# Kernel optimization log

Measured on AMD Instinct MI355X. Metric: run time of the kernel, lower is better.

## Reference

```python
import jax, jax.numpy as jnp
import numpy as np

N = 8192
IN_F = 512
OUT_F = 64
ALPHA = 0.2  # LeakyReLU negative slope
NEG_INF = -9e15


def setup_inputs() -> dict:
    key = jax.random.key(0)
    k1, k2, k3, k4 = jax.random.split(key, 4)
    inp = jax.random.normal(k1, (N, IN_F), dtype=jnp.float32)
    adj = jax.random.randint(k2, (N, N), 0, 2, dtype=jnp.int32)
    W = jax.random.normal(k3, (IN_F, OUT_F), dtype=jnp.float32) * (1.414 * (6.0 / (IN_F + OUT_F)) ** 0.5)
    a = jax.random.normal(k4, (2 * OUT_F, 1), dtype=jnp.float32) * (1.414 * (6.0 / (2 * OUT_F + 1)) ** 0.5)
    return {"input": inp, "adj": adj, "W": W, "a": a}


def reference(input, adj, W, a):
    h = input @ W                      # [N, F]
    F_ = h.shape[1]
    # e_ij = leakyrelu(a[:F].h_i + a[F:].h_j)  (equivalent to the concat form)
    f_src = h @ a[:F_, 0]              # [N]
    f_dst = h @ a[F_:, 0]              # [N]
    e = jax.nn.leaky_relu(f_src[:, None] + f_dst[None, :], negative_slope=ALPHA)  # [N, N]
    att = jnp.where(adj > 0, e, jnp.float32(NEG_INF))
    att = jax.nn.softmax(att, axis=1)  # dropout p is inert in eval mode
    h_prime = att @ h                  # [N, F]
    return jax.nn.elu(h_prime)         # concat=True
```

## Files before the change

kernel.cpp:

```cpp
#include <hip/hip_runtime.h>

#define N_NODES 8192
#define IN_F 512
#define OUT_F 64
#define LOG2E 1.4426950408889634f

typedef short bf16x8 __attribute__((ext_vector_type(8)));
typedef float f32x4 __attribute__((ext_vector_type(4)));
typedef int i32x4 __attribute__((ext_vector_type(4)));

__global__ __launch_bounds__(256) void k_gemm(const float* __restrict__ input,
                                              const float* __restrict__ W,
                                              const float* __restrict__ a,
                                              unsigned short* __restrict__ hT,
                                              float* __restrict__ fsrcL,
                                              float* __restrict__ fdstL) {
  const int lane = threadIdx.x & 63;
  const int wv = threadIdx.x >> 6;
  const int r0 = blockIdx.x * 4;
  const int row = r0 + wv;
  const float* inrow = input + (size_t)row * IN_F;
  const int c = lane;
  float acc = 0.f;
  for (int k = 0; k < IN_F; k += 4) {
    float4 x = *(const float4*)(inrow + k);
    acc += x.x * W[(k + 0) * OUT_F + c];
    acc += x.y * W[(k + 1) * OUT_F + c];
    acc += x.z * W[(k + 2) * OUT_F + c];
    acc += x.w * W[(k + 3) * OUT_F + c];
  }
  float vs = acc * a[c];
  float vd = acc * a[OUT_F + c];
#pragma unroll
  for (int off = 32; off > 0; off >>= 1) {
    vs += __shfl_xor(vs, off, 64);
    vd += __shfl_xor(vd, off, 64);
  }
  if (lane == 0) {
    fsrcL[row] = vs * LOG2E;
    fdstL[row] = vd * LOG2E;
  }
  __shared__ float hs[4][64];
  hs[wv][c] = acc;
  __syncthreads();
  if (threadIdx.x < 64) {
    const int cc = threadIdx.x;
    unsigned u0 = __float_as_uint(hs[0][cc]) + 0x8000u;
    unsigned u1 = __float_as_uint(hs[1][cc]) + 0x8000u;
    unsigned u2 = __float_as_uint(hs[2][cc]) + 0x8000u;
    unsigned u3 = __float_as_uint(hs[3][cc]) + 0x8000u;
    uint2 pk;
    pk.x = __builtin_amdgcn_perm(u1, u0, 0x07060302u);
    pk.y = __builtin_amdgcn_perm(u3, u2, 0x07060302u);
    *(uint2*)(hT + (size_t)cc * N_NODES + r0) = pk;
  }
}

__global__ __launch_bounds__(256) void k_prep(const float* __restrict__ fdstL,
                                              float* __restrict__ ML,
                                              float* __restrict__ E1,
                                              float* __restrict__ E2) {
  float m = -3.0e38f;
  for (int i = threadIdx.x; i < N_NODES; i += 256) {
    float v = fdstL[i];
    E1[i] = __builtin_amdgcn_exp2f(v);
    E2[i] = __builtin_amdgcn_exp2f(0.2f * v);
    m = fmaxf(m, v);
  }
#pragma unroll
  for (int off = 32; off > 0; off >>= 1) m = fmaxf(m, __shfl_xor(m, off, 64));
  __shared__ float sm[4];
  if ((threadIdx.x & 63) == 0) sm[threadIdx.x >> 6] = m;
  __syncthreads();
  if (threadIdx.x == 0) ML[0] = fmaxf(fmaxf(sm[0], sm[1]), fmaxf(sm[2], sm[3]));
}

__global__ __launch_bounds__(512) void k_attn(const int* __restrict__ adj,
                                              const unsigned short* __restrict__ hT,
                                              const float* __restrict__ fsrcL,
                                              const float* __restrict__ MLp,
                                              const float* __restrict__ E1,
                                              const float* __restrict__ E2,
                                              float* __restrict__ out) {
  const int lane = threadIdx.x & 63;
  const int wv = threadIdx.x >> 6;
  const int i0 = blockIdx.x * 16;
  const int m = lane & 15;
  const int g = lane >> 4;

  const float MLv = MLp[0];
  const float fs = fsrcL[i0 + m];
  const float xm = fs + MLv;
  const float mL = fmaxf(xm, 0.2f * xm);
  const float S1 = __builtin_amdgcn_exp2f(fs - mL);
  const float S2 = __builtin_amdgcn_exp2f(0.2f * fs - mL);
  const float Ti = __builtin_amdgcn_exp2f(-fs);

  f32x4 acc0{}, acc1{}, acc2{}, acc3{}, acc4{};
  union { unsigned w[4]; bf16x8 v; } ones;
  ones.w[0] = ones.w[1] = ones.w[2] = ones.w[3] = 0x3F803F80u;

  const int* adjrow = adj + (size_t)(i0 + m) * N_NODES;
  const unsigned short* hT0 = hT + (size_t)m * N_NODES;

  const int jbeg = wv * (N_NODES / 8);
  for (int j0 = jbeg; j0 < jbeg + (N_NODES / 8); j0 += 64) {
#pragma unroll
    for (int s = 0; s < 2; s++) {
      const int jb = j0 + s * 32 + g * 8;
      i32x4 a0 = __builtin_nontemporal_load((const i32x4*)(adjrow + jb));
      i32x4 a1 = __builtin_nontemporal_load((const i32x4*)(adjrow + jb) + 1);
      float4 e1a = *(const float4*)(E1 + jb);
      float4 e1b = *(const float4*)(E1 + jb + 4);
      float4 e2a = *(const float4*)(E2 + jb);
      float4 e2b = *(const float4*)(E2 + jb + 4);
      bf16x8 b0 = *(const bf16x8*)(hT0 + jb);
      bf16x8 b1 = *(const bf16x8*)(hT0 + (size_t)16 * N_NODES + jb);
      bf16x8 b2 = *(const bf16x8*)(hT0 + (size_t)32 * N_NODES + jb);
      bf16x8 b3 = *(const bf16x8*)(hT0 + (size_t)48 * N_NODES + jb);

      const int av[8] = {a0.x, a0.y, a0.z, a0.w, a1.x, a1.y, a1.z, a1.w};
      const float e1v[8] = {e1a.x, e1a.y, e1a.z, e1a.w, e1b.x, e1b.y, e1b.z, e1b.w};
      const float e2v[8] = {e2a.x, e2a.y, e2a.z, e2a.w, e2b.x, e2b.y, e2b.z, e2b.w};
      unsigned u[8];
#pragma unroll
      for (int t = 0; t < 8; t++) {
        float p = (e1v[t] >= Ti) ? e1v[t] * S1 : e2v[t] * S2;
        p = av[t] ? p : 0.0f;
        u[t] = __float_as_uint(p) + 0x8000u;
      }
      union { unsigned w[4]; bf16x8 v; } pc;
      pc.w[0] = __builtin_amdgcn_perm(u[1], u[0], 0x07060302u);
      pc.w[1] = __builtin_amdgcn_perm(u[3], u[2], 0x07060302u);
      pc.w[2] = __builtin_amdgcn_perm(u[5], u[4], 0x07060302u);
      pc.w[3] = __builtin_amdgcn_perm(u[7], u[6], 0x07060302u);

      acc0 = __builtin_amdgcn_mfma_f32_16x16x32_bf16(pc.v, b0, acc0, 0, 0, 0);
      acc1 = __builtin_amdgcn_mfma_f32_16x16x32_bf16(pc.v, b1, acc1, 0, 0, 0);
      acc2 = __builtin_amdgcn_mfma_f32_16x16x32_bf16(pc.v, b2, acc2, 0, 0, 0);
      acc3 = __builtin_amdgcn_mfma_f32_16x16x32_bf16(pc.v, b3, acc3, 0, 0, 0);
      acc4 = __builtin_amdgcn_mfma_f32_16x16x32_bf16(pc.v, ones.v, acc4, 0, 0, 0);
    }
  }

  __shared__ float accbuf[8][16][64];
  __shared__ float lbuf[8][16];
#pragma unroll
  for (int r = 0; r < 4; r++) {
    accbuf[wv][g * 4 + r][0 + m]  = acc0[r];
    accbuf[wv][g * 4 + r][16 + m] = acc1[r];
    accbuf[wv][g * 4 + r][32 + m] = acc2[r];
    accbuf[wv][g * 4 + r][48 + m] = acc3[r];
  }
  if ((lane & 15) == 0) {
#pragma unroll
    for (int r = 0; r < 4; r++) lbuf[wv][g * 4 + r] = acc4[r];
  }
  __syncthreads();

#pragma unroll
  for (int q = 0; q < 2; q++) {
    int idx = q * 512 + threadIdx.x;
    int r = idx >> 6, c = idx & 63;
    float ssum = 0.f, l = 0.f;
#pragma unroll
    for (int w = 0; w < 8; w++) {
      ssum += accbuf[w][r][c];
      l += lbuf[w][r];
    }
    float v = ssum / l;
    out[(size_t)(i0 + r) * OUT_F + c] =
        v > 0.f ? v : __builtin_amdgcn_exp2f(v * LOG2E) - 1.f;
  }
}

extern "C" void kernel_launch(void* const* d_in, const int* in_sizes, int n_in,
                              void* d_out, int out_size, void* d_ws, size_t ws_size,
                              hipStream_t stream) {
  const float* input = (const float*)d_in[0];
  const int* adj = (const int*)d_in[1];
  const float* W = (const float*)d_in[2];
  const float* a = (const float*)d_in[3];
  float* out = (float*)d_out;

  char* ws = (char*)d_ws;
  unsigned short* hT = (unsigned short*)ws;
  float* fsrcL = (float*)(ws + (1u << 20));
  float* fdstL = (float*)(ws + (1u << 20) + 32 * 1024);
  float* ML = (float*)(ws + (1u << 20) + 64 * 1024);
  float* E1 = (float*)(ws + (1u << 20) + 128 * 1024);
  float* E2 = (float*)(ws + (1u << 20) + 160 * 1024);

  k_gemm<<<N_NODES / 4, 256, 0, stream>>>(input, W, a, hT, fsrcL, fdstL);
  k_prep<<<1, 256, 0, stream>>>(fdstL, ML, E1, E2);
  k_attn<<<N_NODES / 16, 512, 0, stream>>>(adj, hT, fsrcL, ML, E1, E2, out);
}
```

Baseline: 516.4 us.

## Compute attention exponent per element instead of precomputed E1/E2 tables

Drops the precomputed exp tables E1/E2 and evaluates leakyrelu and exp2 per edge inside the attention loop, reading only fdst. This halves the per-column vector loads and removes the ones-MFMA used for the row sum, which becomes a scalar accumulation plus two shuffles. The adj loads also lose their nontemporal hint. The cost is one transcendental exp per element, for a kernel that is dominated by streaming the 256MB adjacency matrix.

```diff
diff --git a/kernel.cpp b/kernel.cpp
--- a/kernel.cpp
+++ b/kernel.cpp
@@ -7,7 +7,6 @@
 
 typedef short bf16x8 __attribute__((ext_vector_type(8)));
 typedef float f32x4 __attribute__((ext_vector_type(4)));
-typedef int i32x4 __attribute__((ext_vector_type(4)));
 
 __global__ __launch_bounds__(256) void k_gemm(const float* __restrict__ input,
                                               const float* __restrict__ W,
@@ -56,17 +55,10 @@
   }
 }
 
-__global__ __launch_bounds__(256) void k_prep(const float* __restrict__ fdstL,
-                                              float* __restrict__ ML,
-                                              float* __restrict__ E1,
-                                              float* __restrict__ E2) {
+__global__ __launch_bounds__(256) void k_max(const float* __restrict__ fdstL,
+                                             float* __restrict__ ML) {
   float m = -3.0e38f;
-  for (int i = threadIdx.x; i < N_NODES; i += 256) {
-    float v = fdstL[i];
-    E1[i] = __builtin_amdgcn_exp2f(v);
-    E2[i] = __builtin_amdgcn_exp2f(0.2f * v);
-    m = fmaxf(m, v);
-  }
+  for (int i = threadIdx.x; i < N_NODES; i += 256) m = fmaxf(m, fdstL[i]);
 #pragma unroll
   for (int off = 32; off > 0; off >>= 1) m = fmaxf(m, __shfl_xor(m, off, 64));
   __shared__ float sm[4];
@@ -78,9 +70,8 @@
 __global__ __launch_bounds__(512) void k_attn(const int* __restrict__ adj,
                                               const unsigned short* __restrict__ hT,
                                               const float* __restrict__ fsrcL,
+                                              const float* __restrict__ fdstL,
                                               const float* __restrict__ MLp,
-                                              const float* __restrict__ E1,
-                                              const float* __restrict__ E2,
                                               float* __restrict__ out) {
   const int lane = threadIdx.x & 63;
   const int wv = threadIdx.x >> 6;
@@ -92,13 +83,9 @@
   const float fs = fsrcL[i0 + m];
   const float xm = fs + MLv;
   const float mL = fmaxf(xm, 0.2f * xm);
-  const float S1 = __builtin_amdgcn_exp2f(fs - mL);
-  const float S2 = __builtin_amdgcn_exp2f(0.2f * fs - mL);
-  const float Ti = __builtin_amdgcn_exp2f(-fs);
 
-  f32x4 acc0{}, acc1{}, acc2{}, acc3{}, acc4{};
-  union { unsigned w[4]; bf16x8 v; } ones;
-  ones.w[0] = ones.w[1] = ones.w[2] = ones.w[3] = 0x3F803F80u;
+  f32x4 acc0{}, acc1{}, acc2{}, acc3{};
+  float lpart = 0.f;
 
   const int* adjrow = adj + (size_t)(i0 + m) * N_NODES;
   const unsigned short* hT0 = hT + (size_t)m * N_NODES;
@@ -108,25 +95,25 @@
 #pragma unroll
     for (int s = 0; s < 2; s++) {
       const int jb = j0 + s * 32 + g * 8;
-      i32x4 a0 = __builtin_nontemporal_load((const i32x4*)(adjrow + jb));
-      i32x4 a1 = __builtin_nontemporal_load((const i32x4*)(adjrow + jb) + 1);
-      float4 e1a = *(const float4*)(E1 + jb);
-      float4 e1b = *(const float4*)(E1 + jb + 4);
-      float4 e2a = *(const float4*)(E2 + jb);
-      float4 e2b = *(const float4*)(E2 + jb + 4);
+      int4 a0 = *(const int4*)(adjrow + jb);
+      int4 a1 = *(const int4*)(adjrow + jb + 4);
+      float4 d0 = *(const float4*)(fdstL + jb);
+      float4 d1 = *(const float4*)(fdstL + jb + 4);
       bf16x8 b0 = *(const bf16x8*)(hT0 + jb);
       bf16x8 b1 = *(const bf16x8*)(hT0 + (size_t)16 * N_NODES + jb);
       bf16x8 b2 = *(const bf16x8*)(hT0 + (size_t)32 * N_NODES + jb);
       bf16x8 b3 = *(const bf16x8*)(hT0 + (size_t)48 * N_NODES + jb);
 
       const int av[8] = {a0.x, a0.y, a0.z, a0.w, a1.x, a1.y, a1.z, a1.w};
-      const float e1v[8] = {e1a.x, e1a.y, e1a.z, e1a.w, e1b.x, e1b.y, e1b.z, e1b.w};
-      const float e2v[8] = {e2a.x, e2a.y, e2a.z, e2a.w, e2b.x, e2b.y, e2b.z, e2b.w};
+      const float dv[8] = {d0.x, d0.y, d0.z, d0.w, d1.x, d1.y, d1.z, d1.w};
       unsigned u[8];
 #pragma unroll
       for (int t = 0; t < 8; t++) {
-        float p = (e1v[t] >= Ti) ? e1v[t] * S1 : e2v[t] * S2;
+        float x = fs + dv[t];
+        float y = fmaxf(x, 0.2f * x) - mL;
+        float p = __builtin_amdgcn_exp2f(y);
         p = av[t] ? p : 0.0f;
+        lpart += p;
         u[t] = __float_as_uint(p) + 0x8000u;
       }
       union { unsigned w[4]; bf16x8 v; } pc;
@@ -139,9 +126,11 @@
       acc1 = __builtin_amdgcn_mfma_f32_16x16x32_bf16(pc.v, b1, acc1, 0, 0, 0);
       acc2 = __builtin_amdgcn_mfma_f32_16x16x32_bf16(pc.v, b2, acc2, 0, 0, 0);
       acc3 = __builtin_amdgcn_mfma_f32_16x16x32_bf16(pc.v, b3, acc3, 0, 0, 0);
-      acc4 = __builtin_amdgcn_mfma_f32_16x16x32_bf16(pc.v, ones.v, acc4, 0, 0, 0);
     }
   }
+
+  lpart += __shfl_xor(lpart, 16, 64);
+  lpart += __shfl_xor(lpart, 32, 64);
 
   __shared__ float accbuf[8][16][64];
   __shared__ float lbuf[8][16];
@@ -152,10 +141,7 @@
     accbuf[wv][g * 4 + r][32 + m] = acc2[r];
     accbuf[wv][g * 4 + r][48 + m] = acc3[r];
   }
-  if ((lane & 15) == 0) {
-#pragma unroll
-    for (int r = 0; r < 4; r++) lbuf[wv][g * 4 + r] = acc4[r];
-  }
+  if (lane < 16) lbuf[wv][lane] = lpart;
   __syncthreads();
 
 #pragma unroll
@@ -188,10 +174,8 @@
   float* fsrcL = (float*)(ws + (1u << 20));
   float* fdstL = (float*)(ws + (1u << 20) + 32 * 1024);
   float* ML = (float*)(ws + (1u << 20) + 64 * 1024);
-  float* E1 = (float*)(ws + (1u << 20) + 128 * 1024);
-  float* E2 = (float*)(ws + (1u << 20) + 160 * 1024);
 
   k_gemm<<<N_NODES / 4, 256, 0, stream>>>(input, W, a, hT, fsrcL, fdstL);
-  k_prep<<<1, 256, 0, stream>>>(fdstL, ML, E1, E2);
-  k_attn<<<N_NODES / 16, 512, 0, stream>>>(adj, hT, fsrcL, ML, E1, E2, out);
+  k_max<<<1, 256, 0, stream>>>(fdstL, ML);
+  k_attn<<<N_NODES / 16, 512, 0, stream>>>(adj, hT, fsrcL, fdstL, ML, out);
 }
```

Result: no change. 511.4 us (-1.0%).
